# Performance work log

Hardware: AMD Instinct MI355X
Metric: run time of the kernel (lower is better)

Reference implementation:

```python
import jax, jax.numpy as jnp
import numpy as np

DIM_X, DIM_Z, D_MODEL, N_HEADS, BATCH = 512, 256, 256, 8, 32


def sinusoidal_pe(seq_len, d_model):
    # standard sinusoidal table, rows indexed by position
    pos = np.arange(seq_len)[:, None].astype(np.float32)
    div = np.exp(np.arange(0, d_model, 2).astype(np.float32) * (-np.log(10000.0) / d_model))
    pe = np.zeros((seq_len, d_model), dtype=np.float32)
    pe[:, 0::2] = np.sin(pos * div)
    pe[:, 1::2] = np.cos(pos * div)
    return jnp.asarray(pe)


def setup_inputs() -> dict:
    key = jax.random.key(0)
    ks = jax.random.split(key, 5)
    state = jax.random.normal(ks[0], (BATCH, D_MODEL, DIM_X), dtype=jnp.float32)
    obs = jax.random.normal(ks[1], (BATCH, D_MODEL, DIM_Z), dtype=jnp.float32)
    Qp = jax.random.uniform(ks[2], (DIM_X, D_MODEL), dtype=jnp.float32)  # torch.rand init
    Wq = jax.random.normal(ks[3], (D_MODEL, D_MODEL), dtype=jnp.float32) / np.sqrt(D_MODEL)
    Wk = jax.random.normal(ks[4], (D_MODEL, D_MODEL), dtype=jnp.float32) / np.sqrt(D_MODEL)
    bq = jnp.zeros((D_MODEL,), dtype=jnp.float32)
    bk = jnp.zeros((D_MODEL,), dtype=jnp.float32)
    return {"state": state, "obs": obs, "Qp": Qp, "Wq": Wq, "bq": bq, "Wk": Wk, "bk": bk}


def reference(state, obs, Qp, Wq, bq, Wk, bk):
    bs, en, dim_x = state.shape
    dim_z = obs.shape[2]
    d_model = Qp.shape[1]
    h = N_HEADS
    hd = d_model // h
    S = dim_x + dim_z

    # mean-center over the ensemble axis
    A = state - jnp.mean(state, axis=1, keepdims=True)   # [bs, en, dim_x]
    Y = obs - jnp.mean(obs, axis=1, keepdims=True)       # [bs, en, dim_z]
    A = jnp.transpose(A, (2, 0, 1))                      # [dim_x, bs, en]
    Y = jnp.transpose(Y, (2, 0, 1))                      # [dim_z, bs, en]

    # positional encoding: batch_first=True quirk -> PE indexed along axis 1 (the bs axis)
    pe = sinusoidal_pe(bs, d_model)[None, :, :]          # [1, bs, d_model]
    query = Qp[:, None, :] + pe                          # [dim_x, bs, d_model] (broadcast of repeat)
    xy = jnp.concatenate([A, Y], axis=0) + pe            # [S, bs, d_model]

    # multi-head attention weights (V / out-proj do not affect returned quantities)
    q = (query @ Wq.T + bq).reshape(dim_x, bs, h, hd)
    k = (xy @ Wk.T + bk).reshape(S, bs, h, hd)
    scores = jnp.einsum('lbhd,sbhd->bhls', q, k) / np.sqrt(hd)  # [bs, h, dim_x, S]

    # fixed structured mask: eye(dim_x) | bottom-padded eye(dim_z)
    p1 = jnp.eye(dim_x, dtype=bool)
    p2 = jnp.concatenate([jnp.zeros((dim_x - dim_z, dim_z), dtype=bool),
                          jnp.eye(dim_z, dtype=bool)], axis=0)
    allow = jnp.concatenate([p1, p2], axis=1)            # [dim_x, S]
    scores = jnp.where(allow[None, None], scores, -jnp.inf)
    atten = jnp.mean(jax.nn.softmax(scores, axis=-1), axis=1)  # average over heads -> [bs, dim_x, S]

    # weighted merge of the ORIGINAL (uncentered) state/obs
    merge = jnp.concatenate([jnp.transpose(state, (0, 2, 1)),
                             jnp.transpose(obs, (0, 2, 1))], axis=1)  # [bs, S, en]
    new_state = jnp.einsum('bls,bse->ble', atten, merge)              # [bs, dim_x, en]
    new_state = jnp.transpose(new_state, (0, 2, 1))                   # [bs, en, dim_x]
    return new_state, atten
```

## Files before the change

### kernel.cpp

```cpp
#include <hip/hip_runtime.h>
#include <stdint.h>
#include <math.h>


#define WS_P    0
#define WS_QWT  8192
#define WS_PQ   73728
#define WS_U    81920
#define WS_V    606208
#define WS_QPT  671744
#define WS_WQT  737280

__global__ void __launch_bounds__(256)
k_tr(const float* __restrict__ Qp, const float* __restrict__ Wq,
     float* __restrict__ ws) {
  __shared__ float tile[32][33];
  int bid = blockIdx.x, t = threadIdx.x;
  const float* src; float* dst; int ti;
  if (bid < 64) { src = Qp + 65536; dst = ws + WS_QPT; ti = bid; }
  else          { src = Wq;         dst = ws + WS_WQT; ti = bid - 64; }
  int tr = ti >> 3, tc = ti & 7;
  int c = t & 31, r0 = t >> 5;
  #pragma unroll
  for (int k = 0; k < 4; ++k) {
    int r = r0 + (k << 3);
    tile[r][c] = src[(size_t)(tr * 32 + r) * 256 + tc * 32 + c];
  }
  __syncthreads();
  #pragma unroll
  for (int k = 0; k < 4; ++k) {
    int r = r0 + (k << 3);
    dst[(size_t)(tc * 32 + r) * 256 + tr * 32 + c] = tile[c][r];
  }
}

__global__ void __launch_bounds__(256)
k_pro(const float* __restrict__ Wq, float* __restrict__ ws) {
  int bid = blockIdx.x, t = threadIdx.x;
  if (bid < 288) {
    __shared__ float lvec[256];
    const float* __restrict__ GT; float* dst;
    if (bid < 256) {
      int d = bid;
      lvec[t] = Wq[(size_t)d * 256 + t];
      GT = ws + WS_QPT; dst = ws + WS_QWT + d * 256;
    } else {
      int b = bid - 256;
      int k2 = t & ~1;
      float div = expf((float)k2 * (-9.210340371976184f / 256.f));
      float a = (float)b * div;
      lvec[t] = (t & 1) ? cosf(a) : sinf(a);
      GT = ws + WS_WQT; dst = ws + WS_PQ + b * 256;
    }
    __syncthreads();
    float acc = 0.f;
    #pragma unroll 8
    for (int e = 0; e < 256; ++e)
      acc += lvec[e] * GT[(e << 8) + t];
    dst[t] = acc;
  } else {
    for (int i = t; i < 8192; i += 256) ws[WS_P + i] = 0.f;
  }
}

__global__ void __launch_bounds__(256)
k_uv(const float* __restrict__ Wk, const float* __restrict__ bq,
     float* __restrict__ ws) {
  int bid = blockIdx.x, t = threadIdx.x;
  if (bid < 2048) {
    int h = bid >> 8, e = bid & 255;
    float acc = 0.f;
#pragma unroll 8
    for (int dd = 0; dd < 32; ++dd) {
      int d = h * 32 + dd;
      acc += ws[WS_QWT + d * 256 + t] * Wk[(size_t)d * 256 + e];
    }
    ws[WS_U + ((h << 8) + e) * 256 + t] = acc;
  } else {
    int idx = bid - 2048, b = idx >> 3, h = idx & 7;
    float acc = 0.f;
#pragma unroll 8
    for (int dd = 0; dd < 32; ++dd) {
      int d = h * 32 + dd;
      acc += (ws[WS_PQ + b * 256 + d] + bq[d]) * Wk[(size_t)d * 256 + t];
    }
    ws[WS_V + ((b << 3) + h) * 256 + t] = acc;
  }
}

__global__ void __launch_bounds__(512)
k_delta(const float* __restrict__ state, const float* __restrict__ obs,
        float* __restrict__ ws) {
  int b = blockIdx.x >> 3, h = blockIdx.x & 7;
  int t = threadIdx.x;
  int q = t >> 6, jg = t & 63;
  __shared__ float vsh[256];
  __shared__ float red[512][17];
  if (t < 256) vsh[t] = ws[WS_V + ((b << 3) + h) * 256 + t];
  __syncthreads();
  const float* __restrict__ Uh = ws + WS_U + (h << 16);
  const float4* sp = (const float4*)(state + (size_t)b * 131072 + 256);
  const float4* op = (const float4*)(obs + (size_t)b * 65536);
  float4 a_sw = make_float4(0.f, 0.f, 0.f, 0.f);
  float4 a_w = a_sw, a_s = a_sw, a_o = a_sw;
  int e0 = q << 5;
  #pragma unroll 4
  for (int ei = 0; ei < 32; ++ei) {
    int e = e0 + ei;
    float4 s4 = sp[e * 128 + jg];
    float4 o4 = op[e * 64 + jg];
    float4 u4 = ((const float4*)(Uh + (e << 8)))[jg];
    float ve = vsh[e];
    float w0 = u4.x + ve, w1 = u4.y + ve, w2 = u4.z + ve, w3 = u4.w + ve;
    a_sw.x += (s4.x - o4.x) * w0;
    a_sw.y += (s4.y - o4.y) * w1;
    a_sw.z += (s4.z - o4.z) * w2;
    a_sw.w += (s4.w - o4.w) * w3;
    a_w.x += w0;   a_w.y += w1;   a_w.z += w2;   a_w.w += w3;
    a_s.x += s4.x; a_s.y += s4.y; a_s.z += s4.z; a_s.w += s4.w;
    a_o.x += o4.x; a_o.y += o4.y; a_o.z += o4.z; a_o.w += o4.w;
  }
  float* rr = red[t];
  rr[0]  = a_sw.x; rr[1]  = a_sw.y; rr[2]  = a_sw.z; rr[3]  = a_sw.w;
  rr[4]  = a_w.x;  rr[5]  = a_w.y;  rr[6]  = a_w.z;  rr[7]  = a_w.w;
  rr[8]  = a_s.x;  rr[9]  = a_s.y;  rr[10] = a_s.z;  rr[11] = a_s.w;
  rr[12] = a_o.x;  rr[13] = a_o.y;  rr[14] = a_o.z;  rr[15] = a_o.w;
  __syncthreads();
  if (t < 64) {
    float r[16];
    #pragma unroll
    for (int k = 0; k < 16; ++k) {
      float acc = red[t][k];
      #pragma unroll
      for (int qq = 1; qq < 8; ++qq) acc += red[(qq << 6) + t][k];
      r[k] = acc;
    }
    #pragma unroll
    for (int k = 0; k < 4; ++k) {
      float delta = r[k] - (r[8 + k] - r[12 + k]) * (1.f / 256.f) * r[4 + k];
      float ph = 1.f / (1.f + __expf(-delta * 0.17677669529663687f));
      atomicAdd(&ws[WS_P + b * 256 + (t << 2) + k], ph);
    }
  }
}

__global__ void __launch_bounds__(256)
k_out(const float* __restrict__ state, const float* __restrict__ obs,
      const float* __restrict__ ws, float* __restrict__ out) {
  int bid = blockIdx.x, t = threadIdx.x;
  if (bid < 4096) {
    int row = (bid << 1) | (t >> 7);
    int tt = t & 127;
    int b = row >> 8;
    float4 sv = ((const float4*)(state + (size_t)row * 512))[tt];
    float4* wrow = (float4*)(out + (size_t)row * 512);
    if (tt < 64) {
      wrow[tt] = sv;
    } else {
      float4 ov = ((const float4*)(obs + (size_t)row * 256))[tt - 64];
      float4 p4 = ((const float4*)(ws + WS_P + b * 256))[tt - 64];
      p4.x *= 0.125f; p4.y *= 0.125f; p4.z *= 0.125f; p4.w *= 0.125f;
      float4 r;
      r.x = p4.x * sv.x + (1.f - p4.x) * ov.x;
      r.y = p4.y * sv.y + (1.f - p4.y) * ov.y;
      r.z = p4.z * sv.z + (1.f - p4.z) * ov.z;
      r.w = p4.w * sv.w + (1.f - p4.w) * ov.w;
      wrow[tt] = r;
    }
  } else {
    int g4 = (bid - 4096) * 256 + t;
    int r = g4 / 192, c = g4 - r * 192;
    int b = r >> 9, l = r & 511;
    int s0 = c << 2;
    float v[4] = {0.f, 0.f, 0.f, 0.f};
    if (l < 256) {
      if (l >= s0 && l < s0 + 4) v[l - s0] = 1.0f;
    } else {
      float p = ws[WS_P + b * 256 + (l - 256)] * 0.125f;
      if (l >= s0 && l < s0 + 4) v[l - s0] = p;
      int s2 = l + 256;
      if (s2 >= s0 && s2 < s0 + 4) v[s2 - s0] = 1.0f - p;
    }
    float4 val; val.x = v[0]; val.y = v[1]; val.z = v[2]; val.w = v[3];
    ((float4*)(out + 4194304))[g4] = val;
  }
}

extern "C" void kernel_launch(void* const* d_in, const int* in_sizes, int n_in,
                              void* d_out, int out_size, void* d_ws, size_t ws_size,
                              hipStream_t stream) {
  const float *state = nullptr, *obs = nullptr, *Qp = nullptr;
  const float *Wq = nullptr, *Wk = nullptr, *bq = nullptr, *bk = nullptr;
  for (int i = 0; i < n_in; ++i) {
    int s = in_sizes[i];
    const float* p = (const float*)d_in[i];
    if      (s == 4194304) state = p;
    else if (s == 2097152) obs = p;
    else if (s == 131072)  Qp = p;
    else if (s == 65536)   { if (!Wq) Wq = p; else Wk = p; }
    else if (s == 256)     { if (!bq) bq = p; else bk = p; }
  }
  (void)bk;
  float* out = (float*)d_out;
  float* ws  = (float*)d_ws;

  k_tr   <<<128,   256, 0, stream>>>(Qp, Wq, ws);
  k_pro  <<<289,   256, 0, stream>>>(Wq, ws);
  k_uv   <<<2304,  256, 0, stream>>>(Wk, bq, ws);
  k_delta<<<256,   512, 0, stream>>>(state, obs, ws);
  k_out  <<<16384, 256, 0, stream>>>(state, obs, ws, out);
}
```

Baseline: 142.3 us.

## Restructure k_delta to tile by column and loop heads in-block, drop atomics

k_delta used to assign one block per (batch, head), reading state/obs once per head and combining heads through atomicAdd into a zeroed P buffer. Now each block owns a 32-column slice for one batch. It loads state−obs into shared memory once, loops over all 8 heads, and writes the head-summed sigmoid directly. This removes the 8x redundant state/obs reads, the atomics, and the zeroing pass in k_pro. In exchange U is read with strided scalar loads instead of float4, and shared-memory use per block grows.

New measurement: 131.2 us. 7.8% less time.

```diff
diff --git a/kernel.cpp b/kernel.cpp
--- a/kernel.cpp
+++ b/kernel.cpp
@@ -37,30 +37,26 @@
 __global__ void __launch_bounds__(256)
 k_pro(const float* __restrict__ Wq, float* __restrict__ ws) {
   int bid = blockIdx.x, t = threadIdx.x;
-  if (bid < 288) {
-    __shared__ float lvec[256];
-    const float* __restrict__ GT; float* dst;
-    if (bid < 256) {
-      int d = bid;
-      lvec[t] = Wq[(size_t)d * 256 + t];
-      GT = ws + WS_QPT; dst = ws + WS_QWT + d * 256;
-    } else {
-      int b = bid - 256;
-      int k2 = t & ~1;
-      float div = expf((float)k2 * (-9.210340371976184f / 256.f));
-      float a = (float)b * div;
-      lvec[t] = (t & 1) ? cosf(a) : sinf(a);
-      GT = ws + WS_WQT; dst = ws + WS_PQ + b * 256;
-    }
-    __syncthreads();
-    float acc = 0.f;
-    #pragma unroll 8
-    for (int e = 0; e < 256; ++e)
-      acc += lvec[e] * GT[(e << 8) + t];
-    dst[t] = acc;
+  __shared__ float lvec[256];
+  const float* __restrict__ GT; float* dst;
+  if (bid < 256) {
+    int d = bid;
+    lvec[t] = Wq[(size_t)d * 256 + t];
+    GT = ws + WS_QPT; dst = ws + WS_QWT + d * 256;
   } else {
-    for (int i = t; i < 8192; i += 256) ws[WS_P + i] = 0.f;
-  }
+    int b = bid - 256;
+    int k2 = t & ~1;
+    float div = expf((float)k2 * (-9.210340371976184f / 256.f));
+    float a = (float)b * div;
+    lvec[t] = (t & 1) ? cosf(a) : sinf(a);
+    GT = ws + WS_WQT; dst = ws + WS_PQ + b * 256;
+  }
+  __syncthreads();
+  float acc = 0.f;
+  #pragma unroll 8
+  for (int e = 0; e < 256; ++e)
+    acc += lvec[e] * GT[(e << 8) + t];
+  dst[t] = acc;
 }
 
 __global__ void __launch_bounds__(256)
@@ -88,59 +84,73 @@
   }
 }
 
-__global__ void __launch_bounds__(512)
+__global__ void __launch_bounds__(256)
 k_delta(const float* __restrict__ state, const float* __restrict__ obs,
         float* __restrict__ ws) {
-  int b = blockIdx.x >> 3, h = blockIdx.x & 7;
+  int b = blockIdx.x >> 3, jt = (blockIdx.x & 7) << 5;
   int t = threadIdx.x;
-  int q = t >> 6, jg = t & 63;
-  __shared__ float vsh[256];
-  __shared__ float red[512][17];
-  if (t < 256) vsh[t] = ws[WS_V + ((b << 3) + h) * 256 + t];
-  __syncthreads();
-  const float* __restrict__ Uh = ws + WS_U + (h << 16);
-  const float4* sp = (const float4*)(state + (size_t)b * 131072 + 256);
-  const float4* op = (const float4*)(obs + (size_t)b * 65536);
-  float4 a_sw = make_float4(0.f, 0.f, 0.f, 0.f);
-  float4 a_w = a_sw, a_s = a_sw, a_o = a_sw;
-  int e0 = q << 5;
-  #pragma unroll 4
-  for (int ei = 0; ei < 32; ++ei) {
-    int e = e0 + ei;
-    float4 s4 = sp[e * 128 + jg];
-    float4 o4 = op[e * 64 + jg];
-    float4 u4 = ((const float4*)(Uh + (e << 8)))[jg];
-    float ve = vsh[e];
-    float w0 = u4.x + ve, w1 = u4.y + ve, w2 = u4.z + ve, w3 = u4.w + ve;
-    a_sw.x += (s4.x - o4.x) * w0;
-    a_sw.y += (s4.y - o4.y) * w1;
-    a_sw.z += (s4.z - o4.z) * w2;
-    a_sw.w += (s4.w - o4.w) * w3;
-    a_w.x += w0;   a_w.y += w1;   a_w.z += w2;   a_w.w += w3;
-    a_s.x += s4.x; a_s.y += s4.y; a_s.z += s4.z; a_s.w += s4.w;
-    a_o.x += o4.x; a_o.y += o4.y; a_o.z += o4.z; a_o.w += o4.w;
-  }
-  float* rr = red[t];
-  rr[0]  = a_sw.x; rr[1]  = a_sw.y; rr[2]  = a_sw.z; rr[3]  = a_sw.w;
-  rr[4]  = a_w.x;  rr[5]  = a_w.y;  rr[6]  = a_w.z;  rr[7]  = a_w.w;
-  rr[8]  = a_s.x;  rr[9]  = a_s.y;  rr[10] = a_s.z;  rr[11] = a_s.w;
-  rr[12] = a_o.x;  rr[13] = a_o.y;  rr[14] = a_o.z;  rr[15] = a_o.w;
-  __syncthreads();
-  if (t < 64) {
-    float r[16];
+  __shared__ float Xs[256][33];
+  __shared__ float Vs[2048];
+  __shared__ float pd[8][8][32];
+  __shared__ float pw[8][8][32];
+  __shared__ float px[8][32];
+  {
+    int es = t >> 3, jq = t & 7;
+    const float* sp = state + (size_t)b * 131072 + 256 + jt + (jq << 2);
+    const float* op = obs   + (size_t)b * 65536  + jt + (jq << 2);
     #pragma unroll
-    for (int k = 0; k < 16; ++k) {
-      float acc = red[t][k];
-      #pragma unroll
-      for (int qq = 1; qq < 8; ++qq) acc += red[(qq << 6) + t][k];
-      r[k] = acc;
-    }
+    for (int k = 0; k < 8; ++k) {
+      int e = es + (k << 5);
+      float4 s4 = *(const float4*)(sp + (size_t)e * 512);
+      float4 o4 = *(const float4*)(op + (size_t)e * 256);
+      float* xr = &Xs[e][jq << 2];
+      xr[0] = s4.x - o4.x; xr[1] = s4.y - o4.y;
+      xr[2] = s4.z - o4.z; xr[3] = s4.w - o4.w;
+    }
+    for (int i = t; i < 2048; i += 256) Vs[i] = ws[WS_V + (b << 11) + i];
+  }
+  __syncthreads();
+  int j = t & 31, eg = t >> 5, e0 = eg << 5;
+  {
+    float ax = 0.f;
     #pragma unroll
-    for (int k = 0; k < 4; ++k) {
-      float delta = r[k] - (r[8 + k] - r[12 + k]) * (1.f / 256.f) * r[4 + k];
-      float ph = 1.f / (1.f + __expf(-delta * 0.17677669529663687f));
-      atomicAdd(&ws[WS_P + b * 256 + (t << 2) + k], ph);
-    }
+    for (int ei = 0; ei < 32; ++ei) ax += Xs[e0 + ei][j];
+    px[eg][j] = ax;
+  }
+  const float* __restrict__ Ub = ws + WS_U + jt + j;
+  #pragma unroll
+  for (int h = 0; h < 8; ++h) {
+    float dacc = 0.f, wacc = 0.f;
+    const float* __restrict__ Uh = Ub + (h << 16) + (e0 << 8);
+    const float* __restrict__ Vh = Vs + (h << 8) + e0;
+    #pragma unroll 16
+    for (int ei = 0; ei < 32; ++ei) {
+      float w = Uh[ei << 8] + Vh[ei];
+      dacc += Xs[e0 + ei][j] * w;
+      wacc += w;
+    }
+    pd[eg][h][j] = dacc;
+    pw[eg][h][j] = wacc;
+  }
+  __syncthreads();
+  int h2 = t >> 5, j2 = t & 31;
+  float D = 0.f, W = 0.f, X = 0.f;
+  #pragma unroll
+  for (int g = 0; g < 8; ++g) {
+    D += pd[g][h2][j2];
+    W += pw[g][h2][j2];
+    X += px[g][j2];
+  }
+  float delta = D - X * (1.f / 256.f) * W;
+  float sig = 1.f / (1.f + __expf(-delta * 0.17677669529663687f));
+  __syncthreads();
+  px[h2][j2] = sig;
+  __syncthreads();
+  if (t < 32) {
+    float acc = 0.f;
+    #pragma unroll
+    for (int h = 0; h < 8; ++h) acc += px[h][t];
+    ws[WS_P + (b << 8) + jt + t] = acc;
   }
 }
 
@@ -205,8 +215,8 @@
   float* ws  = (float*)d_ws;
 
   k_tr   <<<128,   256, 0, stream>>>(Qp, Wq, ws);
-  k_pro  <<<289,   256, 0, stream>>>(Wq, ws);
+  k_pro  <<<288,   256, 0, stream>>>(Wq, ws);
   k_uv   <<<2304,  256, 0, stream>>>(Wk, bq, ws);
-  k_delta<<<256,   512, 0, stream>>>(state, obs, ws);
+  k_delta<<<256,   256, 0, stream>>>(state, obs, ws);
   k_out  <<<16384, 256, 0, stream>>>(state, obs, ws, out);
 }
```
